# Optimization experiments

Measured on AMD Instinct MI355X. Metric: run time of the kernel, lower is better.

The kernel has to match this reference:

```python
import jax, jax.numpy as jnp
import numpy as np

THETA = 10000.0

def _rope(x, pos):
    # x: [b, h, s, hd]; pos: [s]
    hd = x.shape[-1]
    inv_freq = 1.0 / (THETA ** (jnp.arange(0, hd, 2, dtype=jnp.float32) / hd))  # [hd/2]
    ang = pos.astype(jnp.float32)[:, None] * inv_freq[None, :]                   # [s, hd/2]
    cos, sin = jnp.cos(ang), jnp.sin(ang)
    x1, x2 = x[..., 0::2], x[..., 1::2]
    r1 = x1 * cos - x2 * sin
    r2 = x1 * sin + x2 * cos
    return jnp.stack([r1, r2], axis=-1).reshape(x.shape)

def setup_inputs() -> dict:
    key = jax.random.key(0)
    ks = jax.random.split(key, 5)
    b, s, d = 2, 2048, 1024
    scale = 0.02
    return {
        "x": jax.random.normal(ks[0], (b, s, d), dtype=jnp.float32),
        "Wq": jax.random.normal(ks[1], (d, d), dtype=jnp.float32) * scale,
        "Wk": jax.random.normal(ks[2], (d, d), dtype=jnp.float32) * scale,
        "Wv": jax.random.normal(ks[3], (d, d), dtype=jnp.float32) * scale,
        "Wo": jax.random.normal(ks[4], (d, d), dtype=jnp.float32) * scale,
    }

def reference(x, Wq, Wk, Wv, Wo):
    b, s, d = x.shape
    n_heads = 16
    hd = d // n_heads

    def split_heads(t):  # [b,s,d] -> [b,h,s,hd]
        return t.reshape(b, s, n_heads, hd).transpose(0, 2, 1, 3)

    q = split_heads(x @ Wq.T)
    k = split_heads(x @ Wk.T)
    v = split_heads(x @ Wv.T)

    pos = jnp.arange(s)
    q = _rope(q, pos)
    k = _rope(k, pos)

    scores = jnp.einsum("bhqd,bhkd->bhqk", q, k) / jnp.sqrt(jnp.float32(hd))
    causal = jnp.tril(jnp.ones((s, s), dtype=bool))
    scores = jnp.where(causal, scores, -jnp.inf)
    attn = jax.nn.softmax(scores, axis=-1)
    ctx = jnp.einsum("bhqk,bhkd->bhqd", attn, v)
    ctx = ctx.transpose(0, 2, 1, 3).reshape(b, s, d)
    return ctx @ Wo.T
```

## Files before the change

### kernel.cpp

```cpp
#include <hip/hip_runtime.h>
#include <math.h>

#define B  2
#define S  2048
#define D  1024
#define NH 16
#define HD 64
#define NROWS (B * S)

#define AS1 __attribute__((address_space(1)))
#define AS3 __attribute__((address_space(3)))
#define GLD16(g, l) __builtin_amdgcn_global_load_lds((const AS1 void*)(g), (AS3 void*)(l), 16, 0, 0)

typedef __attribute__((ext_vector_type(8))) short short8;
typedef __attribute__((ext_vector_type(4))) float floatx4;

#define MFMA16(a, b, c) __builtin_amdgcn_mfma_f32_16x16x32_bf16((a), (b), (c), 0, 0, 0)

__device__ inline float fexp2(float x) { return __builtin_amdgcn_exp2f(x); }

__device__ inline unsigned short f2bf(float f) {
    union { float f; unsigned int u; } v; v.f = f;
    unsigned int u = v.u;
    u += 0x7fffu + ((u >> 16) & 1);
    return (unsigned short)(u >> 16);
}

__device__ inline unsigned int pack2bf(float a, float b) {
    unsigned int ua = __float_as_uint(a) + 0x8000u;
    unsigned int ub = __float_as_uint(b) + 0x8000u;
    return __builtin_amdgcn_perm(ub, ua, 0x07060302u);
}

__global__ __launch_bounds__(256) void cvt_kernel(
    const float* __restrict__ x,  const float* __restrict__ Wq,
    const float* __restrict__ Wk, const float* __restrict__ Wv,
    const float* __restrict__ Wo,
    unsigned short* __restrict__ xb,  unsigned short* __restrict__ wqb,
    unsigned short* __restrict__ wkb, unsigned short* __restrict__ wvb,
    unsigned short* __restrict__ wob, float2* __restrict__ tab)
{
    size_t idx = (size_t)blockIdx.x * 256 + threadIdx.x;
    if (idx >= (2u << 20)) {
        int tt = (int)(idx - (2u << 20));
        int j  = tt >> 9;
        int s0 = (tt & 511) << 2;
        float invf = fexp2(-(float)j * (13.287712379549449f / 32.0f));
        #pragma unroll
        for (int p = 0; p < 4; ++p) {
            float sn, cs;
            __sincosf((float)(s0 + p) * invf, &sn, &cs);
            tab[j * 2048 + s0 + p] = make_float2(cs, sn);
        }
        return;
    }
    const float* src; unsigned short* dst; size_t off;
    if (idx < (1u << 20)) { src = x; dst = xb; off = idx << 2; }
    else {
        size_t r = idx - (1u << 20);
        int w = (int)(r >> 18);
        off = (r & ((1u << 18) - 1)) << 2;
        src = (w == 0) ? Wq : (w == 1) ? Wk : (w == 2) ? Wv : Wo;
        dst = (w == 0) ? wqb : (w == 1) ? wkb : (w == 2) ? wvb : wob;
    }
    float4 f = *(const float4*)(src + off);
    ushort4 o;
    o.x = f2bf(f.x); o.y = f2bf(f.y); o.z = f2bf(f.z); o.w = f2bf(f.w);
    *(ushort4*)(dst + off) = o;
}

#define G2STAGE(Abase, Bbase, kk, AD, BD)                                      \
{                                                                              \
    GLD16(Abase + (size_t)rowS        * D + (kk) + koS, AD + t * 8);           \
    GLD16(Abase + (size_t)(rowS + 64) * D + (kk) + koS, AD + 2048 + t * 8);    \
    GLD16(Bbase + (size_t)rowS        * D + (kk) + koS, BD + t * 8);           \
    GLD16(Bbase + (size_t)(rowS + 64) * D + (kk) + koS, BD + 2048 + t * 8);    \
}

#define G2COMP(AC, BC)                                                         \
{                                                                              \
    short8 a[4], b[4];                                                         \
    _Pragma("unroll")                                                          \
    for (int mi = 0; mi < 4; ++mi)                                             \
        a[mi] = *(const short8*)&AC[(wr * 64 + mi * 16 + lm) * 32 + quad * 8]; \
    _Pragma("unroll")                                                          \
    for (int ni = 0; ni < 4; ++ni)                                             \
        b[ni] = *(const short8*)&BC[(wc * 64 + ni * 16 + lm) * 32 + quad * 8]; \
    _Pragma("unroll")                                                          \
    for (int mi = 0; mi < 4; ++mi)                                             \
        _Pragma("unroll")                                                      \
        for (int ni = 0; ni < 4; ++ni)                                         \
            acc[mi][ni] = MFMA16(b[ni], a[mi], acc[mi][ni]);      \
}

__global__ __launch_bounds__(256, 3) void gemm_qkv_mfma(
    const unsigned short* __restrict__ xb,
    const unsigned short* __restrict__ wqb,
    const unsigned short* __restrict__ wkb,
    const unsigned short* __restrict__ wvb,
    const float2* __restrict__ tab,
    unsigned short* __restrict__ Qo, unsigned short* __restrict__ Ko,
    unsigned short* __restrict__ Vo)
{
    __shared__ short As0[128 * 32];
    __shared__ short As1[128 * 32];
    __shared__ short Bs0[128 * 32];
    __shared__ short Bs1[128 * 32];

    const int t    = threadIdx.x;
    const int wave = t >> 6, lane = t & 63;
    const int lm   = lane & 15, quad = lane >> 4;
    const int wr   = wave >> 1, wc = wave & 1;
    const int rowS = t >> 2;
    const int koS  = (t & 3) << 3;

    const int i0  = blockIdx.x * 128;
    const int by  = blockIdx.y;
    const int mat = by >> 3;
    const int j0  = (by & 7) * 128;
    const unsigned short* __restrict__ W = (mat == 0) ? wqb : (mat == 1) ? wkb : wvb;
    unsigned short* __restrict__ out = (mat == 0) ? Qo : (mat == 1) ? Ko : Vo;

    const unsigned short* Abase = xb + (size_t)i0 * D;
    const unsigned short* Bbase = W  + (size_t)j0 * D;

    floatx4 acc[4][4] = {};

    G2STAGE(Abase, Bbase, 0, As0, Bs0);
    __syncthreads();
    for (int k0 = 0; k0 < D; k0 += 64) {
        G2STAGE(Abase, Bbase, k0 + 32, As1, Bs1);
        G2COMP(As0, Bs0);
        __syncthreads();
        if (k0 + 64 < D) G2STAGE(Abase, Bbase, k0 + 64, As0, Bs0);
        G2COMP(As1, Bs1);
        __syncthreads();
    }

    const int h = (j0 + wc * 64) >> 6;
    if (mat < 2) {
        #pragma unroll
        for (int mi = 0; mi < 4; ++mi) {
            const int mg = i0 + wr * 64 + mi * 16 + lm;
            const int si = mg & (S - 1), bb = mg >> 11;
            unsigned short* orow = out + ((size_t)(bb * NH + h) * S + si) * HD;
            #pragma unroll
            for (int ni = 0; ni < 4; ++ni) {
                const int dim0 = ni * 16 + quad * 4;
                const int j = dim0 >> 1;
                float2 t0 = tab[j * 2048 + si];
                float2 t1 = tab[(j + 1) * 2048 + si];
                floatx4 v = acc[mi][ni];
                float r0 = v[0] * t0.x - v[1] * t0.y;
                float r1 = v[0] * t0.y + v[1] * t0.x;
                float r2 = v[2] * t1.x - v[3] * t1.y;
                float r3 = v[2] * t1.y + v[3] * t1.x;
                if (mat == 0) {
                    r0 *= 0.1803368801111204f; r1 *= 0.1803368801111204f;
                    r2 *= 0.1803368801111204f; r3 *= 0.1803368801111204f;
                }
                ushort4 pk;
                pk.x = f2bf(r0); pk.y = f2bf(r1);
                pk.z = f2bf(r2); pk.w = f2bf(r3);
                *(ushort4*)(orow + dim0) = pk;
            }
        }
    } else {
        #pragma unroll
        for (int mi = 0; mi < 4; ++mi) {
            const int mg = i0 + wr * 64 + mi * 16 + lm;
            const int si = mg & (S - 1), bb = mg >> 11;
            unsigned short* vb = out + (size_t)(bb * NH + h) * HD * S + si;
            #pragma unroll
            for (int ni = 0; ni < 4; ++ni) {
                const int d0 = ni * 16 + quad * 4;
                #pragma unroll
                for (int p = 0; p < 4; ++p)
                    vb[(size_t)(d0 + p) * S] = f2bf(acc[mi][ni][p]);
            }
        }
    }
}

#define GSTAGE(Abase, Bbase, kk, AD, BD)                                       \
{                                                                              \
    GLD16(Abase + (size_t)rowA  * D + (kk) + koA,  AD + cA  * 8);              \
    GLD16(Bbase + (size_t)rowB0 * D + (kk) + koB0, BD + cB0 * 8);              \
    GLD16(Bbase + (size_t)rowB1 * D + (kk) + koB1, BD + cB1 * 8);              \
}

#define GCOMP(AC, BC)                                                          \
{                                                                              \
    short8 a[4], b[2];                                                         \
    _Pragma("unroll")                                                          \
    for (int mi = 0; mi < 4; ++mi)                                             \
        a[mi] = *(const short8*)&AC[(mi * 16 + lm) * 32 + quad * 8];           \
    _Pragma("unroll")                                                          \
    for (int ni = 0; ni < 2; ++ni)                                             \
        b[ni] = *(const short8*)&BC[(wave * 32 + ni * 16 + lm) * 32 + quad * 8]; \
    _Pragma("unroll")                                                          \
    for (int mi = 0; mi < 4; ++mi)                                             \
        _Pragma("unroll")                                                      \
        for (int ni = 0; ni < 2; ++ni)                                         \
            acc[mi][ni] = MFMA16(b[ni], a[mi], acc[mi][ni]);      \
}

#define GEMM_PREAMBLE                                                          \
    const int t    = threadIdx.x;                                              \
    const int wave = t >> 6, lane = t & 63;                                    \
    const int lm   = lane & 15, quad = lane >> 4;                              \
    const int cA   = wave * 64 + lane;                                         \
    const int rowA = cA >> 2,  koA  = (cA & 3) << 3;                           \
    const int cB0  = wave * 128 + lane;                                        \
    const int rowB0 = cB0 >> 2, koB0 = (cB0 & 3) << 3;                         \
    const int cB1  = cB0 + 64;                                                 \
    const int rowB1 = cB1 >> 2, koB1 = (cB1 & 3) << 3;

#define GEMM_KLOOP(Abase, Bbase)                                               \
    GSTAGE(Abase, Bbase, 0, As0, Bs0);                                         \
    __syncthreads();                                                           \
    for (int k0 = 0; k0 < D; k0 += 64) {                                       \
        GSTAGE(Abase, Bbase, k0 + 32, As1, Bs1);                               \
        GCOMP(As0, Bs0);                                                       \
        __syncthreads();                                                       \
        if (k0 + 64 < D) GSTAGE(Abase, Bbase, k0 + 64, As0, Bs0);              \
        GCOMP(As1, Bs1);                                                       \
        __syncthreads();                                                       \
    }

__global__ __launch_bounds__(256) void gemm_out_mfma(
    const unsigned short* __restrict__ Cb,
    const unsigned short* __restrict__ wob,
    float* __restrict__ out)
{
    __shared__ short As0[64 * 32];
    __shared__ short As1[64 * 32];
    __shared__ short Bs0[128 * 32];
    __shared__ short Bs1[128 * 32];

    GEMM_PREAMBLE
    const int i0 = blockIdx.x * 64;
    const int j0 = blockIdx.y * 128;

    const unsigned short* Abase = Cb  + (size_t)i0 * D;
    const unsigned short* Bbase = wob + (size_t)j0 * D;

    floatx4 acc[4][2] = {};
    GEMM_KLOOP(Abase, Bbase)

    #pragma unroll
    for (int mi = 0; mi < 4; ++mi) {
        const int mg = i0 + mi * 16 + lm;
        float* orow = out + (size_t)mg * D;
        #pragma unroll
        for (int ni = 0; ni < 2; ++ni) {
            const int ng = j0 + wave * 32 + ni * 16 + quad * 4;
            *(floatx4*)(orow + ng) = acc[mi][ni];
        }
    }
}

#define ATTN_STEP(KC, VC, KN, VN)                                              \
{                                                                              \
    _Pragma("unroll")                                                          \
    for (int i = 0; i < 2; ++i) {                                              \
        int c = t + i * 256;                                                   \
        int row = c >> 3;                                                      \
        int dkc = (c & 7) ^ (row & 7);                                         \
        GLD16(Kg + (size_t)(k0n + row) * HD + dkc * 8, &KN[0][0] + c * 8);     \
        GLD16(Vg + (size_t)row * S + k0n + dkc * 8,    &VN[0][0] + c * 8);     \
    }                                                                          \
    short8 kb0[4], kb1[4];                                                     \
    _Pragma("unroll")                                                          \
    for (int nt = 0; nt < 4; ++nt) {                                           \
        kb0[nt] = *(const short8*)&KC[nt * 16 + lm][(quad ^ sw) * 8];          \
        kb1[nt] = *(const short8*)&KC[nt * 16 + lm][((4 + quad) ^ sw) * 8];    \
    }                                                                          \
    floatx4 sc[4];                                                             \
    _Pragma("unroll")                                                          \
    for (int nt = 0; nt < 4; ++nt) {                                           \
        floatx4 s = {0.f, 0.f, 0.f, 0.f};                                      \
        s = MFMA16(kb0[nt], qa0, s);                \
        s = MFMA16(kb1[nt], qa1, s);                                           \
        sc[nt] = s;                                                            \
    }                                                                          \
    if (diag) {                                                                \
        _Pragma("unroll")                                                      \
        for (int nt = 0; nt < 4; ++nt)                                         \
            _Pragma("unroll")                                                  \
            for (int r = 0; r < 4; ++r) {                                      \
                float pe = fexp2(sc[nt][r]);                                   \
                if (nt * 16 + quad * 4 + r > 16 * wave + lm) pe = 0.0f;        \
                sc[nt][r] = pe;                                                \
            }                                                                  \
    } else {                                                                   \
        _Pragma("unroll")                                                      \
        for (int nt = 0; nt < 4; ++nt)                                         \
            _Pragma("unroll")                                                  \
            for (int r = 0; r < 4; ++r)                                        \
                sc[nt][r] = fexp2(sc[nt][r]);                                  \
    }                                                                          \
    _Pragma("unroll")                                                          \
    for (int nt = 0; nt < 4; ++nt) {                                           \
        uint2 pk;                                                              \
        pk.x = pack2bf(sc[nt][0], sc[nt][1]);                                  \
        pk.y = pack2bf(sc[nt][2], sc[nt][3]);                                  \
        int cp = (nt * 4 + quad) ^ psw;                                        \
        *(uint2*)&Ps[16 * wave + lm][cp * 4] = pk;                             \
    }                                                                          \
    short8 pa0 = *(const short8*)&Ps[16 * wave + lm][((quad * 2) ^ psw) * 4];  \
    short8 pa1 = *(const short8*)&Ps[16 * wave + lm][((8 + quad * 2) ^ psw) * 4]; \
    osum = MFMA16(pa0, vones, osum);         \
    osum = MFMA16(pa1, vones, osum);                                           \
    _Pragma("unroll")                                                          \
    for (int nt = 0; nt < 4; ++nt) {                                           \
        short8 vb0 = *(const short8*)&VC[nt * 16 + lm][(quad ^ sw) * 8];       \
        short8 vb1 = *(const short8*)&VC[nt * 16 + lm][((4 + quad) ^ sw) * 8]; \
        o[nt] = MFMA16(pa0, vb0, o[nt]);                                       \
        o[nt] = MFMA16(pa1, vb1, o[nt]);                                       \
    }                                                                          \
    __syncthreads();                                                           \
}

__global__ __launch_bounds__(256, 4) void attn_mfma(
    const unsigned short* __restrict__ Qb,
    const unsigned short* __restrict__ Kb,
    const unsigned short* __restrict__ Vt,
    unsigned short* __restrict__ Cb)
{
    __shared__ unsigned short Ks0[64][64];
    __shared__ unsigned short Ks1[64][64];
    __shared__ unsigned short Vs0[64][64];
    __shared__ unsigned short Vs1[64][64];
    __shared__ unsigned short Ps[64][64];

    const int t    = threadIdx.x;
    const int lane = t & 63, wave = t >> 6;
    const int lm   = lane & 15, quad = lane >> 4;
    const int sw   = lm & 7;
    const int psw  = (lm & 7) << 1;

    const int b     = blockIdx.x;
    const int bh    = b & 31;
    const int f     = (b >> 5) & 7;
    const int round = b >> 8;
    int qt;
    if      (round == 0) qt = f;
    else if (round == 1) qt = 15 - f;
    else if (round == 2) qt = 16 + f;
    else                 qt = 31 - f;
    const int q0 = qt * 64;

    const unsigned short* Qg = Qb + (size_t)bh * S * HD;
    const unsigned short* Kg = Kb + (size_t)bh * S * HD;
    const unsigned short* Vg = Vt + (size_t)bh * HD * S;

    short8 qa0 = *(const short8*)(Qg + (size_t)(q0 + 16 * wave + lm) * HD + quad * 8);
    short8 qa1 = *(const short8*)(Qg + (size_t)(q0 + 16 * wave + lm) * HD + 32 + quad * 8);

    short8 vones;
    #pragma unroll
    for (int i = 0; i < 8; ++i) vones[i] = (short)0x3F80;

    #pragma unroll
    for (int i = 0; i < 2; ++i) {
        int c = t + i * 256;
        int row = c >> 3;
        int dkc = (c & 7) ^ (row & 7);
        GLD16(Kg + (size_t)row * HD + dkc * 8, &Ks0[0][0] + c * 8);
        GLD16(Vg + (size_t)row * S + dkc * 8,  &Vs0[0][0] + c * 8);
    }

    floatx4 o[4] = {};
    floatx4 osum = {};

    __syncthreads();

    for (int kt = 0; kt <= qt; ++kt) {
        const int k0n = (kt + 1) * 64;
        const bool diag = (kt == qt);
        if ((kt & 1) == 0) ATTN_STEP(Ks0, Vs0, Ks1, Vs1)
        else               ATTN_STEP(Ks1, Vs1, Ks0, Vs0)
    }

    const int h = bh & (NH - 1), bb = bh >> 4;
    #pragma unroll
    for (int r = 0; r < 4; ++r) {
        float inv = 1.0f / osum[r];
        size_t row = (size_t)bb * S + q0 + 16 * wave + quad * 4 + r;
        #pragma unroll
        for (int nt = 0; nt < 4; ++nt)
            Cb[row * D + h * HD + nt * 16 + lm] = f2bf(o[nt][r] * inv);
    }
}

extern "C" void kernel_launch(void* const* d_in, const int* in_sizes, int n_in,
                              void* d_out, int out_size, void* d_ws, size_t ws_size,
                              hipStream_t stream) {
    (void)in_sizes; (void)n_in; (void)out_size; (void)ws_size;
    const float* x  = (const float*)d_in[0];
    const float* Wq = (const float*)d_in[1];
    const float* Wk = (const float*)d_in[2];
    const float* Wv = (const float*)d_in[3];
    const float* Wo = (const float*)d_in[4];
    float* out = (float*)d_out;

    char* w = (char*)d_ws;
    unsigned short* Qb  = (unsigned short*)(w);
    unsigned short* Kb  = (unsigned short*)(w + (((size_t)8)  << 20));
    unsigned short* Vtb = (unsigned short*)(w + (((size_t)16) << 20));
    unsigned short* Cb  = (unsigned short*)(w + (((size_t)24) << 20));
    unsigned short* xb  = (unsigned short*)(w + (((size_t)32) << 20));
    unsigned short* wqb = (unsigned short*)(w + (((size_t)40) << 20));
    unsigned short* wkb = (unsigned short*)(w + (((size_t)42) << 20));
    unsigned short* wvb = (unsigned short*)(w + (((size_t)44) << 20));
    unsigned short* wob = (unsigned short*)(w + (((size_t)46) << 20));
    float2*         tab = (float2*)(w + (((size_t)48) << 20));

    cvt_kernel<<<8256, 256, 0, stream>>>(x, Wq, Wk, Wv, Wo,
                                         xb, wqb, wkb, wvb, wob, tab);

    dim3 g1(NROWS / 128, 24);
    gemm_qkv_mfma<<<g1, 256, 0, stream>>>(xb, wqb, wkb, wvb, tab, Qb, Kb, Vtb);

    attn_mfma<<<1024, 256, 0, stream>>>(Qb, Kb, Vtb, Cb);

    dim3 g3(NROWS / 64, D / 128);
    gemm_out_mfma<<<g3, 256, 0, stream>>>(Cb, wob, out);
}
```

Baseline: 169.1 us.

## Software-pipeline attention: compute next tile's QK scores during current PV step

Restructures the attention loop so the QK^T MFMAs for tile kt+1 are issued while the exp/pack/PV work of tile kt is in flight, with K prefetched two tiles ahead and V one tile ahead. The intent is to overlap the exp/bf16-pack latency with independent MFMA work and hide the load latency. It adds register pressure (an extra score array) under a 4-blocks-per-SM launch bound, and makes the buffer indexing more intricate.

```diff
diff --git a/kernel.cpp b/kernel.cpp
--- a/kernel.cpp
+++ b/kernel.cpp
@@ -260,78 +260,14 @@
     }
 }
 
-#define ATTN_STEP(KC, VC, KN, VN)                                              \
-{                                                                              \
-    _Pragma("unroll")                                                          \
-    for (int i = 0; i < 2; ++i) {                                              \
-        int c = t + i * 256;                                                   \
-        int row = c >> 3;                                                      \
-        int dkc = (c & 7) ^ (row & 7);                                         \
-        GLD16(Kg + (size_t)(k0n + row) * HD + dkc * 8, &KN[0][0] + c * 8);     \
-        GLD16(Vg + (size_t)row * S + k0n + dkc * 8,    &VN[0][0] + c * 8);     \
-    }                                                                          \
-    short8 kb0[4], kb1[4];                                                     \
-    _Pragma("unroll")                                                          \
-    for (int nt = 0; nt < 4; ++nt) {                                           \
-        kb0[nt] = *(const short8*)&KC[nt * 16 + lm][(quad ^ sw) * 8];          \
-        kb1[nt] = *(const short8*)&KC[nt * 16 + lm][((4 + quad) ^ sw) * 8];    \
-    }                                                                          \
-    floatx4 sc[4];                                                             \
-    _Pragma("unroll")                                                          \
-    for (int nt = 0; nt < 4; ++nt) {                                           \
-        floatx4 s = {0.f, 0.f, 0.f, 0.f};                                      \
-        s = MFMA16(kb0[nt], qa0, s);                \
-        s = MFMA16(kb1[nt], qa1, s);                                           \
-        sc[nt] = s;                                                            \
-    }                                                                          \
-    if (diag) {                                                                \
-        _Pragma("unroll")                                                      \
-        for (int nt = 0; nt < 4; ++nt)                                         \
-            _Pragma("unroll")                                                  \
-            for (int r = 0; r < 4; ++r) {                                      \
-                float pe = fexp2(sc[nt][r]);                                   \
-                if (nt * 16 + quad * 4 + r > 16 * wave + lm) pe = 0.0f;        \
-                sc[nt][r] = pe;                                                \
-            }                                                                  \
-    } else {                                                                   \
-        _Pragma("unroll")                                                      \
-        for (int nt = 0; nt < 4; ++nt)                                         \
-            _Pragma("unroll")                                                  \
-            for (int r = 0; r < 4; ++r)                                        \
-                sc[nt][r] = fexp2(sc[nt][r]);                                  \
-    }                                                                          \
-    _Pragma("unroll")                                                          \
-    for (int nt = 0; nt < 4; ++nt) {                                           \
-        uint2 pk;                                                              \
-        pk.x = pack2bf(sc[nt][0], sc[nt][1]);                                  \
-        pk.y = pack2bf(sc[nt][2], sc[nt][3]);                                  \
-        int cp = (nt * 4 + quad) ^ psw;                                        \
-        *(uint2*)&Ps[16 * wave + lm][cp * 4] = pk;                             \
-    }                                                                          \
-    short8 pa0 = *(const short8*)&Ps[16 * wave + lm][((quad * 2) ^ psw) * 4];  \
-    short8 pa1 = *(const short8*)&Ps[16 * wave + lm][((8 + quad * 2) ^ psw) * 4]; \
-    osum = MFMA16(pa0, vones, osum);         \
-    osum = MFMA16(pa1, vones, osum);                                           \
-    _Pragma("unroll")                                                          \
-    for (int nt = 0; nt < 4; ++nt) {                                           \
-        short8 vb0 = *(const short8*)&VC[nt * 16 + lm][(quad ^ sw) * 8];       \
-        short8 vb1 = *(const short8*)&VC[nt * 16 + lm][((4 + quad) ^ sw) * 8]; \
-        o[nt] = MFMA16(pa0, vb0, o[nt]);                                       \
-        o[nt] = MFMA16(pa1, vb1, o[nt]);                                       \
-    }                                                                          \
-    __syncthreads();                                                           \
-}
-
 __global__ __launch_bounds__(256, 4) void attn_mfma(
     const unsigned short* __restrict__ Qb,
     const unsigned short* __restrict__ Kb,
     const unsigned short* __restrict__ Vt,
     unsigned short* __restrict__ Cb)
 {
-    __shared__ unsigned short Ks0[64][64];
-    __shared__ unsigned short Ks1[64][64];
-    __shared__ unsigned short Vs0[64][64];
-    __shared__ unsigned short Vs1[64][64];
+    __shared__ unsigned short Ks[2][64][64];
+    __shared__ unsigned short Vs[2][64][64];
     __shared__ unsigned short Ps[64][64];
 
     const int t    = threadIdx.x;
@@ -367,20 +303,107 @@
         int c = t + i * 256;
         int row = c >> 3;
         int dkc = (c & 7) ^ (row & 7);
-        GLD16(Kg + (size_t)row * HD + dkc * 8, &Ks0[0][0] + c * 8);
-        GLD16(Vg + (size_t)row * S + dkc * 8,  &Vs0[0][0] + c * 8);
+        GLD16(Kg + (size_t)row * HD + dkc * 8,        &Ks[0][0][0] + c * 8);
+        GLD16(Vg + (size_t)row * S + dkc * 8,         &Vs[0][0][0] + c * 8);
+        GLD16(Kg + (size_t)(64 + row) * HD + dkc * 8, &Ks[1][0][0] + c * 8);
     }
 
     floatx4 o[4] = {};
     floatx4 osum = {};
+    floatx4 sc[4], scn[4];
+    #pragma unroll
+    for (int nt = 0; nt < 4; ++nt) scn[nt] = floatx4{0.f, 0.f, 0.f, 0.f};
 
     __syncthreads();
 
+    #pragma unroll
+    for (int nt = 0; nt < 4; ++nt) {
+        short8 kb0 = *(const short8*)&Ks[0][nt * 16 + lm][(quad ^ sw) * 8];
+        short8 kb1 = *(const short8*)&Ks[0][nt * 16 + lm][((4 + quad) ^ sw) * 8];
+        floatx4 s = {0.f, 0.f, 0.f, 0.f};
+        s = MFMA16(kb0, qa0, s);
+        s = MFMA16(kb1, qa1, s);
+        sc[nt] = s;
+    }
+
     for (int kt = 0; kt <= qt; ++kt) {
-        const int k0n = (kt + 1) * 64;
-        const bool diag = (kt == qt);
-        if ((kt & 1) == 0) ATTN_STEP(Ks0, Vs0, Ks1, Vs1)
-        else               ATTN_STEP(Ks1, Vs1, Ks0, Vs0)
+        const int pb = kt & 1;
+
+        if (kt + 2 <= qt) {
+            const int k0n = (kt + 2) * 64;
+            #pragma unroll
+            for (int i = 0; i < 2; ++i) {
+                int c = t + i * 256;
+                int row = c >> 3;
+                int dkc = (c & 7) ^ (row & 7);
+                GLD16(Kg + (size_t)(k0n + row) * HD + dkc * 8, &Ks[pb][0][0] + c * 8);
+            }
+        }
+        if (kt + 1 <= qt) {
+            const int k0v = (kt + 1) * 64;
+            #pragma unroll
+            for (int i = 0; i < 2; ++i) {
+                int c = t + i * 256;
+                int row = c >> 3;
+                int dkc = (c & 7) ^ (row & 7);
+                GLD16(Vg + (size_t)row * S + k0v + dkc * 8, &Vs[pb ^ 1][0][0] + c * 8);
+            }
+        }
+
+        if (kt == qt) {
+            #pragma unroll
+            for (int nt = 0; nt < 4; ++nt)
+                #pragma unroll
+                for (int r = 0; r < 4; ++r) {
+                    float pe = fexp2(sc[nt][r]);
+                    if (nt * 16 + quad * 4 + r > 16 * wave + lm) pe = 0.0f;
+                    sc[nt][r] = pe;
+                }
+        } else {
+            #pragma unroll
+            for (int nt = 0; nt < 4; ++nt)
+                #pragma unroll
+                for (int r = 0; r < 4; ++r)
+                    sc[nt][r] = fexp2(sc[nt][r]);
+        }
+
+        #pragma unroll
+        for (int nt = 0; nt < 4; ++nt) {
+            uint2 pk;
+            pk.x = pack2bf(sc[nt][0], sc[nt][1]);
+            pk.y = pack2bf(sc[nt][2], sc[nt][3]);
+            int cp = (nt * 4 + quad) ^ psw;
+            *(uint2*)&Ps[16 * wave + lm][cp * 4] = pk;
+        }
+
+        if (kt < qt) {
+            #pragma unroll
+            for (int nt = 0; nt < 4; ++nt) {
+                short8 kb0 = *(const short8*)&Ks[pb ^ 1][nt * 16 + lm][(quad ^ sw) * 8];
+                short8 kb1 = *(const short8*)&Ks[pb ^ 1][nt * 16 + lm][((4 + quad) ^ sw) * 8];
+                floatx4 s = {0.f, 0.f, 0.f, 0.f};
+                s = MFMA16(kb0, qa0, s);
+                s = MFMA16(kb1, qa1, s);
+                scn[nt] = s;
+            }
+        }
+
+        short8 pa0 = *(const short8*)&Ps[16 * wave + lm][((quad * 2) ^ psw) * 4];
+        short8 pa1 = *(const short8*)&Ps[16 * wave + lm][((8 + quad * 2) ^ psw) * 4];
+        osum = MFMA16(pa0, vones, osum);
+        osum = MFMA16(pa1, vones, osum);
+        #pragma unroll
+        for (int nt = 0; nt < 4; ++nt) {
+            short8 vb0 = *(const short8*)&Vs[pb][nt * 16 + lm][(quad ^ sw) * 8];
+            short8 vb1 = *(const short8*)&Vs[pb][nt * 16 + lm][((4 + quad) ^ sw) * 8];
+            o[nt] = MFMA16(pa0, vb0, o[nt]);
+            o[nt] = MFMA16(pa1, vb1, o[nt]);
+        }
+
+        __syncthreads();
+
+        #pragma unroll
+        for (int nt = 0; nt < 4; ++nt) sc[nt] = scn[nt];
     }
 
     const int h = bh & (NH - 1), bb = bh >> 4;
```

Result: no change. 168.0 us (-0.7%).

## Keep softmax probabilities in registers via 16x16x16 MFMA instead of LDS round-trip

Applied to the files above, without the earlier changes.

The attention step no longer writes P to a shared-memory tile and reads it back. The score accumulator layout is reused directly as the A operand of 16x16x16 bf16 MFMAs, and V fragments are loaded in matching 4-element pieces. This drops the Ps LDS buffer, so launch bounds go up to 5 blocks per SM, and the prefetch of the next K/V tile is skipped after the last needed tile. The trade-off is twice as many smaller MFMA instructions and more, narrower LDS reads of V, plus an inline-asm fallback with manual nops if the builtin is missing.

```diff
diff --git a/kernel.cpp b/kernel.cpp
--- a/kernel.cpp
+++ b/kernel.cpp
@@ -13,9 +13,22 @@
 #define GLD16(g, l) __builtin_amdgcn_global_load_lds((const AS1 void*)(g), (AS3 void*)(l), 16, 0, 0)
 
 typedef __attribute__((ext_vector_type(8))) short short8;
+typedef __attribute__((ext_vector_type(4))) short short4v;
 typedef __attribute__((ext_vector_type(4))) float floatx4;
 
 #define MFMA16(a, b, c) __builtin_amdgcn_mfma_f32_16x16x32_bf16((a), (b), (c), 0, 0, 0)
+
+#if __has_builtin(__builtin_amdgcn_mfma_f32_16x16x16bf16_1k)
+#define MFMAK16(a, b, c) __builtin_amdgcn_mfma_f32_16x16x16bf16_1k((a), (b), (c), 0, 0, 0)
+#else
+__device__ inline floatx4 mfmak16_asm(short4v a, short4v b, floatx4 c) {
+    floatx4 d;
+    asm volatile("s_nop 1\n\ts_nop 1\n\tv_mfma_f32_16x16x16_bf16 %0, %1, %2, %3\n\ts_nop 1"
+                 : "=v"(d) : "v"(a), "v"(b), "v"(c));
+    return d;
+}
+#define MFMAK16(a, b, c) mfmak16_asm((a), (b), (c))
+#endif
 
 __device__ inline float fexp2(float x) { return __builtin_amdgcn_exp2f(x); }
 
@@ -262,26 +275,24 @@
 
 #define ATTN_STEP(KC, VC, KN, VN)                                              \
 {                                                                              \
-    _Pragma("unroll")                                                          \
-    for (int i = 0; i < 2; ++i) {                                              \
-        int c = t + i * 256;                                                   \
-        int row = c >> 3;                                                      \
-        int dkc = (c & 7) ^ (row & 7);                                         \
-        GLD16(Kg + (size_t)(k0n + row) * HD + dkc * 8, &KN[0][0] + c * 8);     \
-        GLD16(Vg + (size_t)row * S + k0n + dkc * 8,    &VN[0][0] + c * 8);     \
-    }                                                                          \
-    short8 kb0[4], kb1[4];                                                     \
-    _Pragma("unroll")                                                          \
-    for (int nt = 0; nt < 4; ++nt) {                                           \
-        kb0[nt] = *(const short8*)&KC[nt * 16 + lm][(quad ^ sw) * 8];          \
-        kb1[nt] = *(const short8*)&KC[nt * 16 + lm][((4 + quad) ^ sw) * 8];    \
+    if (k0n <= qt * 64) {                                                      \
+        _Pragma("unroll")                                                      \
+        for (int i = 0; i < 2; ++i) {                                          \
+            int c = t + i * 256;                                               \
+            int row = c >> 3;                                                  \
+            int dkc = (c & 7) ^ (row & 7);                                     \
+            GLD16(Kg + (size_t)(k0n + row) * HD + dkc * 8, &KN[0][0] + c * 8); \
+            GLD16(Vg + (size_t)row * S + k0n + dkc * 8,    &VN[0][0] + c * 8); \
+        }                                                                      \
     }                                                                          \
     floatx4 sc[4];                                                             \
     _Pragma("unroll")                                                          \
     for (int nt = 0; nt < 4; ++nt) {                                           \
+        short8 kb0 = *(const short8*)&KC[nt * 16 + lm][(quad ^ sw) * 8];       \
+        short8 kb1 = *(const short8*)&KC[nt * 16 + lm][((4 + quad) ^ sw) * 8]; \
         floatx4 s = {0.f, 0.f, 0.f, 0.f};                                      \
-        s = MFMA16(kb0[nt], qa0, s);                \
-        s = MFMA16(kb1[nt], qa1, s);                                           \
+        s = MFMA16(kb0, qa0, s);                    \
+        s = MFMA16(kb1, qa1, s);                                               \
         sc[nt] = s;                                                            \
     }                                                                          \
     if (diag) {                                                                \
@@ -300,29 +311,30 @@
             for (int r = 0; r < 4; ++r)                                        \
                 sc[nt][r] = fexp2(sc[nt][r]);                                  \
     }                                                                          \
+    short4v pa[4];                                                             \
     _Pragma("unroll")                                                          \
     for (int nt = 0; nt < 4; ++nt) {                                           \
-        uint2 pk;                                                              \
-        pk.x = pack2bf(sc[nt][0], sc[nt][1]);                                  \
-        pk.y = pack2bf(sc[nt][2], sc[nt][3]);                                  \
-        int cp = (nt * 4 + quad) ^ psw;                                        \
-        *(uint2*)&Ps[16 * wave + lm][cp * 4] = pk;                             \
+        union { uint2 u; short4v s; } cv;                                      \
+        cv.u.x = pack2bf(sc[nt][0], sc[nt][1]);                                \
+        cv.u.y = pack2bf(sc[nt][2], sc[nt][3]);                                \
+        pa[nt] = cv.s;                                                         \
     }                                                                          \
-    short8 pa0 = *(const short8*)&Ps[16 * wave + lm][((quad * 2) ^ psw) * 4];  \
-    short8 pa1 = *(const short8*)&Ps[16 * wave + lm][((8 + quad * 2) ^ psw) * 4]; \
-    osum = MFMA16(pa0, vones, osum);         \
-    osum = MFMA16(pa1, vones, osum);                                           \
-    _Pragma("unroll")                                                          \
-    for (int nt = 0; nt < 4; ++nt) {                                           \
-        short8 vb0 = *(const short8*)&VC[nt * 16 + lm][(quad ^ sw) * 8];       \
-        short8 vb1 = *(const short8*)&VC[nt * 16 + lm][((4 + quad) ^ sw) * 8]; \
-        o[nt] = MFMA16(pa0, vb0, o[nt]);                                       \
-        o[nt] = MFMA16(pa1, vb1, o[nt]);                                       \
+    _Pragma("unroll")                                                          \
+    for (int nt = 0; nt < 4; ++nt)                                             \
+        osum = MFMAK16(pa[nt], vones4, osum);   \
+    _Pragma("unroll")                                                          \
+    for (int ntd = 0; ntd < 4; ++ntd) {                                        \
+        _Pragma("unroll")                                                      \
+        for (int ntk = 0; ntk < 4; ++ntk) {                                    \
+            short4v vb = *(const short4v*)&VC[ntd * 16 + lm]                   \
+                [((2 * ntk + (quad >> 1)) ^ sw) * 8 + (quad & 1) * 4];         \
+            o[ntd] = MFMAK16(pa[ntk], vb, o[ntd]);                             \
+        }                                                                      \
     }                                                                          \
     __syncthreads();                                                           \
 }
 
-__global__ __launch_bounds__(256, 4) void attn_mfma(
+__global__ __launch_bounds__(256, 5) void attn_mfma(
     const unsigned short* __restrict__ Qb,
     const unsigned short* __restrict__ Kb,
     const unsigned short* __restrict__ Vt,
@@ -332,13 +344,11 @@
     __shared__ unsigned short Ks1[64][64];
     __shared__ unsigned short Vs0[64][64];
     __shared__ unsigned short Vs1[64][64];
-    __shared__ unsigned short Ps[64][64];
 
     const int t    = threadIdx.x;
     const int lane = t & 63, wave = t >> 6;
     const int lm   = lane & 15, quad = lane >> 4;
     const int sw   = lm & 7;
-    const int psw  = (lm & 7) << 1;
 
     const int b     = blockIdx.x;
     const int bh    = b & 31;
@@ -358,9 +368,9 @@
     short8 qa0 = *(const short8*)(Qg + (size_t)(q0 + 16 * wave + lm) * HD + quad * 8);
     short8 qa1 = *(const short8*)(Qg + (size_t)(q0 + 16 * wave + lm) * HD + 32 + quad * 8);
 
-    short8 vones;
+    short4v vones4;
     #pragma unroll
-    for (int i = 0; i < 8; ++i) vones[i] = (short)0x3F80;
+    for (int i = 0; i < 4; ++i) vones4[i] = (short)0x3F80;
 
     #pragma unroll
     for (int i = 0; i < 2; ++i) {
```

Result: slower. 177.3 us (+4.8%).
